# Kernel optimization log

Measured on AMD Instinct MI355X. Metric: run time of the kernel, lower is better.

Reference implementation:

```python
import jax, jax.numpy as jnp
import numpy as np

MAX_K = 32


def _label_count_segment(vals):
    """Faithful port of MetaKNetwork._get_label_count_segment (relative=False).
    vals: [B,S,K] int labels of the K nearest neighbors.
    Returns [B,S,K] int: number of distinct nonzero labels in prefixes vals[:, :, :i+1].
    """
    K = vals.shape[-1]
    # triu mask with diagonal=1: row i keeps vals[0..i], masks the rest to -1
    mask = jnp.triu(jnp.ones((K, K), dtype=bool), k=1)
    ev = jnp.where(mask, jnp.int32(-1), vals[..., None, :].astype(jnp.int32))  # [B,S,K,K]
    ls = jnp.sort(ev, axis=-1)
    # zero out consecutive duplicates (keep first occurrence), exactly as the torch code
    dedup = ls[..., 1:] * (ls[..., 1:] != ls[..., :-1]).astype(jnp.int32)
    ls = jnp.concatenate([ls[..., :1], dedup], axis=-1)
    counts = jnp.sum(ls != 0, axis=-1)  # [B,S,K]
    # rows 0..K-2 contain at least one -1 sentinel which was counted once -> subtract 1
    counts = counts - (jnp.arange(K) < K - 1).astype(counts.dtype)
    return counts


def _mlp2(x, w1, b1, w2, b2):
    # nn.Sequential(Linear, Tanh, Linear); weights stored as [in, out]
    return jnp.tanh(x @ w1 + b1) @ w2 + b2


def setup_inputs() -> dict:
    key = jax.random.key(0)
    ks = jax.random.split(key, 10)
    B, S, K = 32, 1024, MAX_K
    mid = 32
    vals = jax.random.randint(ks[0], (B, S, K), 0, 100, dtype=jnp.int32)
    distances = jax.random.uniform(ks[1], (B, S, K), dtype=jnp.float32)
    s = 0.1
    return {
        "vals": vals,
        "distances": distances,
        # distance_fc2: Linear(2K, 32) -> Tanh -> Linear(32, 2)
        "fc2_w1": jax.random.normal(ks[2], (2 * K, mid), dtype=jnp.float32) * s,
        "fc2_b1": jnp.zeros((mid,), jnp.float32),
        "fc2_w2": jax.random.normal(ks[3], (mid, 2), dtype=jnp.float32) * s,
        "fc2_b2": jnp.zeros((2,), jnp.float32),
        # distance_fc1: Linear(2, 4) -> Tanh -> Linear(4, 1)
        "fc1_w1": jax.random.normal(ks[4], (2, 4), dtype=jnp.float32) * s,
        "fc1_b1": jnp.zeros((4,), jnp.float32),
        "fc1_w2": jax.random.normal(ks[5], (4, 1), dtype=jnp.float32) * s,
        "fc1_b2": jnp.zeros((1,), jnp.float32),
    }


def reference(vals, distances, fc2_w1, fc2_b1, fc2_w2, fc2_b2, fc1_w1, fc1_b1, fc1_w2, fc1_b2):
    label_counts = _label_count_segment(vals)  # [B,S,K]
    # original detaches both features before feeding the heads
    net_in = jnp.concatenate(
        [jax.lax.stop_gradient(distances), jax.lax.stop_gradient(label_counts.astype(jnp.float32))],
        axis=-1,
    )  # [B,S,2K]
    fc2_out = _mlp2(net_in, fc2_w1, fc2_b1, fc2_w2, fc2_b2)  # [B,S,2]
    fc1_out = _mlp2(fc2_out, fc1_w1, fc1_b1, fc1_w2, fc1_b2)  # [B,S,1]
    return jnp.concatenate([fc2_out, fc1_out], axis=-1)  # [B,S,3]
```

## Files before the change

kernel.cpp:

```cpp
#include <hip/hip_runtime.h>

#define K 32
#define RPB 64

__device__ __forceinline__ float fast_tanh(float x) {
    x = fminf(20.0f, fmaxf(-20.0f, x));
    float t = __builtin_amdgcn_exp2f(x * 2.8853900817779268f);
    return (t - 1.0f) * __builtin_amdgcn_rcpf(t + 1.0f);
}

__global__ __launch_bounds__(RPB) void metak_kernel(
    const int* __restrict__ vals, const float* __restrict__ dist,
    const float* __restrict__ w1, const float* __restrict__ b1,
    const float* __restrict__ w2, const float* __restrict__ b2,
    const float* __restrict__ fw1, const float* __restrict__ fb1,
    const float* __restrict__ fw2, const float* __restrict__ fb2,
    float* __restrict__ out)
{
    __shared__ float ld_d[RPB * 33];
    __shared__ int   ld_v[RPB * 33];
    const int tid = threadIdx.x;
    const int base = blockIdx.x * (RPB * K);

    #pragma unroll
    for (int it = 0; it < K; ++it) {
        int e = it * 64 + tid;
        int r = e >> 5, c = e & 31;
        ld_d[r * 33 + c] = dist[base + e];
        ld_v[r * 33 + c] = vals[base + e];
    }
    __syncthreads();

    float d[K]; int v[K];
    #pragma unroll
    for (int k = 0; k < K; ++k) {
        d[k] = ld_d[tid * 33 + k];
        v[k] = ld_v[tid * 33 + k];
    }

    float c[K];
    unsigned long long lo = 0ull, hi = 0ull;
    int cnt = 0;
    #pragma unroll
    for (int k = 0; k < K; ++k) {
        int x = v[k];
        if (x != 0) {
            if ((unsigned)x < 128u) {
                unsigned long long bit = 1ull << (x & 63);
                if (x < 64) { cnt += (lo & bit) ? 0 : 1; lo |= bit; }
                else        { cnt += (hi & bit) ? 0 : 1; hi |= bit; }
            } else {
                bool dup = false;
                #pragma unroll
                for (int j = 0; j < K; ++j) dup = dup || (j < k && v[j] == x);
                cnt += dup ? 0 : 1;
            }
        }
        c[k] = (float)cnt;
    }

    float h[32];
    #pragma unroll
    for (int j = 0; j < 32; ++j) h[j] = b1[j];
    #pragma unroll
    for (int i = 0; i < 32; ++i) {
        float x = d[i];
        #pragma unroll
        for (int j = 0; j < 32; ++j) h[j] = fmaf(x, w1[i * 32 + j], h[j]);
    }
    #pragma unroll
    for (int i = 0; i < 32; ++i) {
        float x = c[i];
        #pragma unroll
        for (int j = 0; j < 32; ++j) h[j] = fmaf(x, w1[(32 + i) * 32 + j], h[j]);
    }

    float o0 = b2[0], o1 = b2[1];
    #pragma unroll
    for (int j = 0; j < 32; ++j) {
        float th = fast_tanh(h[j]);
        o0 = fmaf(th, w2[j * 2 + 0], o0);
        o1 = fmaf(th, w2[j * 2 + 1], o1);
    }

    float o2 = fb2[0];
    #pragma unroll
    for (int m = 0; m < 4; ++m) {
        float g = fast_tanh(fb1[m] + o0 * fw1[m] + o1 * fw1[4 + m]);
        o2 = fmaf(g, fw2[m], o2);
    }

    const int row = blockIdx.x * RPB + tid;
    out[row * 3 + 0] = o0;
    out[row * 3 + 1] = o1;
    out[row * 3 + 2] = o2;
}

extern "C" void kernel_launch(void* const* d_in, const int* in_sizes, int n_in,
                              void* d_out, int out_size, void* d_ws, size_t ws_size,
                              hipStream_t stream) {
    const int*   vals = (const int*)d_in[0];
    const float* dist = (const float*)d_in[1];
    const float* w1   = (const float*)d_in[2];
    const float* b1   = (const float*)d_in[3];
    const float* w2   = (const float*)d_in[4];
    const float* b2   = (const float*)d_in[5];
    const float* fw1  = (const float*)d_in[6];
    const float* fb1  = (const float*)d_in[7];
    const float* fw2  = (const float*)d_in[8];
    const float* fb2  = (const float*)d_in[9];
    float* out = (float*)d_out;

    const int rows   = in_sizes[0] / K;
    const int blocks = rows / RPB;

    metak_kernel<<<blocks, RPB, 0, stream>>>(vals, dist, w1, b1, w2, b2,
                                             fw1, fb1, fw2, fb2, out);
}
```

Measured before the change: 100.3 us.

## Split each row's hidden layer across four threads with shuffle reduction

Each row is now handled by four threads instead of one. Each thread computes 8 of the 32 hidden units, and the partial fc2 outputs are combined with xor shuffles. Blocks grow to 256 threads while still covering 64 rows. The aim is to cut per-thread FMA work and register pressure and to raise occupancy. The cost is that the label-count scan and the shared-memory row loads are now done four times per row.

```diff
diff --git a/kernel.cpp b/kernel.cpp
--- a/kernel.cpp
+++ b/kernel.cpp
@@ -1,7 +1,9 @@
 #include <hip/hip_runtime.h>
 
 #define K 32
-#define RPB 64
+#define TPR 4
+#define BLOCK 256
+#define RPB (BLOCK / TPR)
 
 __device__ __forceinline__ float fast_tanh(float x) {
     x = fminf(20.0f, fmaxf(-20.0f, x));
@@ -9,7 +11,7 @@
     return (t - 1.0f) * __builtin_amdgcn_rcpf(t + 1.0f);
 }
 
-__global__ __launch_bounds__(RPB) void metak_kernel(
+__global__ __launch_bounds__(BLOCK) void metak_kernel(
     const int* __restrict__ vals, const float* __restrict__ dist,
     const float* __restrict__ w1, const float* __restrict__ b1,
     const float* __restrict__ w2, const float* __restrict__ b2,
@@ -19,12 +21,15 @@
 {
     __shared__ float ld_d[RPB * 33];
     __shared__ int   ld_v[RPB * 33];
-    const int tid = threadIdx.x;
+
+    const int tid  = threadIdx.x;
+    const int sub  = tid & (TPR - 1);
+    const int rloc = tid >> 2;
     const int base = blockIdx.x * (RPB * K);
 
     #pragma unroll
-    for (int it = 0; it < K; ++it) {
-        int e = it * 64 + tid;
+    for (int it = 0; it < 8; ++it) {
+        int e = it * BLOCK + tid;
         int r = e >> 5, c = e & 31;
         ld_d[r * 33 + c] = dist[base + e];
         ld_v[r * 33 + c] = vals[base + e];
@@ -34,8 +39,8 @@
     float d[K]; int v[K];
     #pragma unroll
     for (int k = 0; k < K; ++k) {
-        d[k] = ld_d[tid * 33 + k];
-        v[k] = ld_v[tid * 33 + k];
+        d[k] = ld_d[rloc * 33 + k];
+        v[k] = ld_v[rloc * 33 + k];
     }
 
     float c[K];
@@ -59,29 +64,34 @@
         c[k] = (float)cnt;
     }
 
-    float h[32];
+    const int j0 = sub * 8;
+    float h[8];
     #pragma unroll
-    for (int j = 0; j < 32; ++j) h[j] = b1[j];
+    for (int j = 0; j < 8; ++j) h[j] = b1[j0 + j];
     #pragma unroll
-    for (int i = 0; i < 32; ++i) {
+    for (int i = 0; i < K; ++i) {
         float x = d[i];
         #pragma unroll
-        for (int j = 0; j < 32; ++j) h[j] = fmaf(x, w1[i * 32 + j], h[j]);
+        for (int j = 0; j < 8; ++j) h[j] = fmaf(x, w1[i * 32 + j0 + j], h[j]);
     }
     #pragma unroll
-    for (int i = 0; i < 32; ++i) {
+    for (int i = 0; i < K; ++i) {
         float x = c[i];
         #pragma unroll
-        for (int j = 0; j < 32; ++j) h[j] = fmaf(x, w1[(32 + i) * 32 + j], h[j]);
+        for (int j = 0; j < 8; ++j) h[j] = fmaf(x, w1[(K + i) * 32 + j0 + j], h[j]);
     }
 
-    float o0 = b2[0], o1 = b2[1];
+    float p0 = 0.0f, p1 = 0.0f;
     #pragma unroll
-    for (int j = 0; j < 32; ++j) {
+    for (int j = 0; j < 8; ++j) {
         float th = fast_tanh(h[j]);
-        o0 = fmaf(th, w2[j * 2 + 0], o0);
-        o1 = fmaf(th, w2[j * 2 + 1], o1);
+        p0 = fmaf(th, w2[(j0 + j) * 2 + 0], p0);
+        p1 = fmaf(th, w2[(j0 + j) * 2 + 1], p1);
     }
+    p0 += __shfl_xor(p0, 1); p0 += __shfl_xor(p0, 2);
+    p1 += __shfl_xor(p1, 1); p1 += __shfl_xor(p1, 2);
+    const float o0 = p0 + b2[0];
+    const float o1 = p1 + b2[1];
 
     float o2 = fb2[0];
     #pragma unroll
@@ -90,10 +100,9 @@
         o2 = fmaf(g, fw2[m], o2);
     }
 
-    const int row = blockIdx.x * RPB + tid;
-    out[row * 3 + 0] = o0;
-    out[row * 3 + 1] = o1;
-    out[row * 3 + 2] = o2;
+    const int row = blockIdx.x * RPB + rloc;
+    float oval = (sub == 0) ? o0 : (sub == 1) ? o1 : o2;
+    if (sub < 3) out[row * 3 + sub] = oval;
 }
 
 extern "C" void kernel_launch(void* const* d_in, const int* in_sizes, int n_in,
@@ -114,6 +123,6 @@
     const int rows   = in_sizes[0] / K;
     const int blocks = rows / RPB;
 
-    metak_kernel<<<blocks, RPB, 0, stream>>>(vals, dist, w1, b1, w2, b2,
-                                             fw1, fb1, fw2, fb2, out);
+    metak_kernel<<<blocks, BLOCK, 0, stream>>>(vals, dist, w1, b1, w2, b2,
+                                               fw1, fb1, fw2, fb2, out);
 }
```

Result: faster. 84.21 us (-16.1%).
